# Kernel tuning notes

Measured on AMD Instinct MI355X. Metric: run time of the kernel, lower is better.

The kernel has to match this reference:

```python
import jax, jax.numpy as jnp
import numpy as np

DIM = 128
B, N = 2, 72


def setup_inputs() -> dict:
    key = jax.random.key(0)
    ks = jax.random.split(key, 6)
    s = 1.0 / np.sqrt(DIM)
    s3 = 1.0 / np.sqrt(3 * DIM)
    return {
        "node_emb": jax.random.normal(ks[0], (B * N, DIM), dtype=jnp.float32),
        "path_emb": jax.random.normal(ks[1], (B, N, N, DIM), dtype=jnp.float32),
        "W_hz": jax.random.uniform(ks[2], (DIM, DIM), minval=-s, maxval=s, dtype=jnp.float32),
        "b_hz": jax.random.uniform(ks[3], (DIM,), minval=-s, maxval=s, dtype=jnp.float32),
        "W_zz": jax.random.uniform(ks[4], (3 * DIM, DIM), minval=-s3, maxval=s3, dtype=jnp.float32),
        "b_zz": jax.random.uniform(ks[5], (DIM,), minval=-s3, maxval=s3, dtype=jnp.float32),
    }


def reference(node_emb, path_emb, W_hz, b_hz, W_zz, b_zz):
    b, n, _, d = path_emb.shape
    # z = W_hz(path_emb)
    z = jnp.einsum('bijd,de->bije', path_emb, W_hz) + b_hz
    # tropical (max-plus) triangle aggregation: out[b,i,j,d] = max_k z[b,i,k,d] + z[b,k,j,d]
    z_conv = jnp.max(z[:, :, :, None, :] + z[:, None, :, :, :], axis=2)  # (b,n,n,d)
    # path_aggr with mode 'max' -> elementwise max of z_conv and z
    z = jnp.maximum(z_conv, z)
    ne = node_emb.reshape(b, n, d)
    n_i = jnp.broadcast_to(ne[:, :, None, :], (b, n, n, d))
    n_j = jnp.broadcast_to(ne[:, None, :, :], (b, n, n, d))
    zc = jnp.concatenate([n_i, z, n_j], axis=-1)  # (b,n,n,3d)
    out = jax.nn.relu(jnp.einsum('bijc,ce->bije', zc, W_zz) + b_zz)
    return out
```

## Files before the change

kernel.cpp:

```cpp
#include <hip/hip_runtime.h>

#define DIM 128
#define NN 72
#define BB 2
#define NROWS (BB*NN*NN)
#define BN (BB*NN)
#define ZBLOCKS (NROWS/16)

__global__ __launch_bounds__(256) void k_phase1(const float* __restrict__ path,
                                                const float* __restrict__ Whz,
                                                const float* __restrict__ bhz,
                                                float* __restrict__ z,
                                                const float* __restrict__ node,
                                                const float* __restrict__ Wzz,
                                                float* __restrict__ P1,
                                                float* __restrict__ P3) {
    __shared__ float rows[16 * DIM];
    const int t = threadIdx.x;

    if (blockIdx.x < ZBLOCKS) {
        const int r0 = blockIdx.x * 16;
        {
            float4* rs = (float4*)rows;
            const float4* pg = (const float4*)(path + r0 * DIM);
            rs[t]       = pg[t];
            rs[t + 256] = pg[t + 256];
        }
        __syncthreads();

        const int e2 = t & 63;
        const int rg = t >> 6;
        float2 bz = *(const float2*)&bhz[2 * e2];
        float2 acc[4];
#pragma unroll
        for (int r = 0; r < 4; r++) acc[r] = bz;

        const float* Wp = Whz + 2 * e2;
        float2 w[4], wn[4];
#pragma unroll
        for (int dd = 0; dd < 4; dd++) w[dd] = *(const float2*)&Wp[dd * DIM];

        for (int d4 = 0; d4 < DIM / 4; d4++) {
            if (d4 < DIM / 4 - 1) {
#pragma unroll
                for (int dd = 0; dd < 4; dd++)
                    wn[dd] = *(const float2*)&Wp[(4 * d4 + 4 + dd) * DIM];
            }
            float4 pr[4];
#pragma unroll
            for (int r = 0; r < 4; r++)
                pr[r] = *(const float4*)&rows[(rg + 4 * r) * DIM + 4 * d4];
#pragma unroll
            for (int dd = 0; dd < 4; dd++)
#pragma unroll
                for (int r = 0; r < 4; r++) {
                    float pv = ((const float*)&pr[r])[dd];
                    acc[r].x = fmaf(pv, w[dd].x, acc[r].x);
                    acc[r].y = fmaf(pv, w[dd].y, acc[r].y);
                }
#pragma unroll
            for (int dd = 0; dd < 4; dd++) w[dd] = wn[dd];
        }
#pragma unroll
        for (int r = 0; r < 4; r++)
            *(float2*)&z[(r0 + rg + 4 * r) * DIM + 2 * e2] = acc[r];
    } else {
        const int r0 = (blockIdx.x - ZBLOCKS) * 8;
        {
            float4* rs = (float4*)rows;
            const float4* ng = (const float4*)(node + r0 * DIM);
            rs[t] = ng[t];
        }
        __syncthreads();
        const int e  = t & 127;
        const int rr = t >> 7;
        float a1[4] = {0.f, 0.f, 0.f, 0.f};
        float a3[4] = {0.f, 0.f, 0.f, 0.f};
        const float* W1 = Wzz + e;
        const float* W3 = Wzz + 2 * DIM * DIM + e;
        for (int d = 0; d < DIM; d++) {
            float w1 = W1[d * DIM];
            float w3 = W3[d * DIM];
#pragma unroll
            for (int s = 0; s < 4; s++) {
                float pv = rows[(rr + 2 * s) * DIM + d];
                a1[s] = fmaf(pv, w1, a1[s]);
                a3[s] = fmaf(pv, w3, a3[s]);
            }
        }
#pragma unroll
        for (int s = 0; s < 4; s++) {
            int m = r0 + rr + 2 * s;
            P1[m * DIM + e] = a1[s];
            P3[m * DIM + e] = a3[s];
        }
    }
}

__global__ __launch_bounds__(256) void k_trop(const float* __restrict__ z,
                                              float* __restrict__ zmax) {
    __shared__ float comb[16 * DIM];
    const int blk = blockIdx.x;
    const int b   = blk / 324;
    const int rem = blk - b * 324;
    const int it  = rem / 18;
    const int jt  = rem - it * 18;
    const int i0 = it * 4, j0 = jt * 4;
    const int t  = threadIdx.x;
    const int d  = t & 127;
    const int ty = t >> 7;
    const float* zb = z + b * NN * NN * DIM;

    float acc[16];
#pragma unroll
    for (int q = 0; q < 16; q++) acc[q] = -3.402823466e38f;

    float zi[4], zj[4], zin[4], zjn[4];
    int k = ty;
#pragma unroll
    for (int a = 0; a < 4; a++) zi[a] = zb[((i0 + a) * NN + k) * DIM + d];
#pragma unroll
    for (int c = 0; c < 4; c++) zj[c] = zb[(k * NN + (j0 + c)) * DIM + d];

    for (int it2 = 0; it2 < NN / 2; it2++) {
        int kn = k + 2;
        if (it2 < NN / 2 - 1) {
#pragma unroll
            for (int a = 0; a < 4; a++) zin[a] = zb[((i0 + a) * NN + kn) * DIM + d];
#pragma unroll
            for (int c = 0; c < 4; c++) zjn[c] = zb[(kn * NN + (j0 + c)) * DIM + d];
        }
#pragma unroll
        for (int a = 0; a < 4; a++)
#pragma unroll
            for (int c = 0; c < 4; c++)
                acc[a * 4 + c] = fmaxf(acc[a * 4 + c], zi[a] + zj[c]);
#pragma unroll
        for (int a = 0; a < 4; a++) { zi[a] = zin[a]; zj[a] = zjn[a]; }
        k = kn;
    }

    if (ty == 1) {
#pragma unroll
        for (int q = 0; q < 16; q++) comb[q * DIM + d] = acc[q];
    }
    __syncthreads();
    if (ty == 0) {
        float* zmb = zmax + b * NN * NN * DIM;
#pragma unroll
        for (int a = 0; a < 4; a++)
#pragma unroll
            for (int c = 0; c < 4; c++) {
                int q = a * 4 + c;
                float m = fmaxf(acc[q], comb[q * DIM + d]);
                int idx = ((i0 + a) * NN + (j0 + c)) * DIM + d;
                zmb[idx] = fmaxf(m, zb[idx]);
            }
    }
}

__global__ __launch_bounds__(256) void k_out(const float* zin,
                                             const float* __restrict__ Wzz,
                                             const float* __restrict__ bzz,
                                             const float* __restrict__ P1,
                                             const float* __restrict__ P3,
                                             float* out) {
    __shared__ float rows[16 * DIM];
    const int t  = threadIdx.x;
    const int r0 = blockIdx.x * 16;
    {
        float4* rs = (float4*)rows;
        const float4* zg = (const float4*)(zin + r0 * DIM);
        rs[t]       = zg[t];
        rs[t + 256] = zg[t + 256];
    }
    __syncthreads();

    const int e2 = t & 63;
    const int rg = t >> 6;
    float2 acc[4];
#pragma unroll
    for (int r = 0; r < 4; r++) acc[r] = make_float2(0.f, 0.f);

    const float* Wp = Wzz + DIM * DIM + 2 * e2;
    float2 w[4], wn[4];
#pragma unroll
    for (int dd = 0; dd < 4; dd++) w[dd] = *(const float2*)&Wp[dd * DIM];

    for (int d4 = 0; d4 < DIM / 4; d4++) {
        if (d4 < DIM / 4 - 1) {
#pragma unroll
            for (int dd = 0; dd < 4; dd++)
                wn[dd] = *(const float2*)&Wp[(4 * d4 + 4 + dd) * DIM];
        }
        float4 pr[4];
#pragma unroll
        for (int r = 0; r < 4; r++)
            pr[r] = *(const float4*)&rows[(rg + 4 * r) * DIM + 4 * d4];
#pragma unroll
        for (int dd = 0; dd < 4; dd++)
#pragma unroll
            for (int r = 0; r < 4; r++) {
                float pv = ((const float*)&pr[r])[dd];
                acc[r].x = fmaf(pv, w[dd].x, acc[r].x);
                acc[r].y = fmaf(pv, w[dd].y, acc[r].y);
            }
#pragma unroll
        for (int dd = 0; dd < 4; dd++) w[dd] = wn[dd];
    }

    float2 bz = *(const float2*)&bzz[2 * e2];
#pragma unroll
    for (int r = 0; r < 4; r++) {
        int row = r0 + rg + 4 * r;
        int bi  = row / NN;
        int b   = row / (NN * NN);
        int j   = row - bi * NN;
        float2 v1 = *(const float2*)&P1[bi * DIM + 2 * e2];
        float2 v3 = *(const float2*)&P3[(b * NN + j) * DIM + 2 * e2];
        float ox = fmaxf(acc[r].x + v1.x + v3.x + bz.x, 0.f);
        float oy = fmaxf(acc[r].y + v1.y + v3.y + bz.y, 0.f);
        *(float2*)&out[row * DIM + 2 * e2] = make_float2(ox, oy);
    }
}

extern "C" void kernel_launch(void* const* d_in, const int* in_sizes, int n_in,
                              void* d_out, int out_size, void* d_ws, size_t ws_size,
                              hipStream_t stream) {
    const float* node = (const float*)d_in[0];
    const float* path = (const float*)d_in[1];
    const float* Whz  = (const float*)d_in[2];
    const float* bhz  = (const float*)d_in[3];
    const float* Wzz  = (const float*)d_in[4];
    const float* bzz  = (const float*)d_in[5];
    float* out = (float*)d_out;

    float* z  = (float*)d_ws;
    float* P1 = z + NROWS * DIM;
    float* P3 = P1 + BN * DIM;
    float* zmax = out;

    hipLaunchKernelGGL(k_phase1, dim3(ZBLOCKS + 18), dim3(256), 0, stream,
                       path, Whz, bhz, z, node, Wzz, P1, P3);
    hipLaunchKernelGGL(k_trop,   dim3(BB * 18 * 18), dim3(256), 0, stream, z, zmax);
    hipLaunchKernelGGL(k_out,    dim3(ZBLOCKS),      dim3(256), 0, stream,
                       zmax, Wzz, bzz, P1, P3, out);
}
```

Before: 114.3 us.

## Fuse three kernels into one persistent kernel with a grid-wide barrier

Merges the projection, tropical max-plus aggregation and output GEMM into one kernel of 648 blocks, separated by a software grid barrier built on an atomic counter. The tropical result tile is kept in shared memory and fed straight into the output projection, so the intermediate zmax no longer goes through global memory. This also removes two kernel launch gaps. In exchange it adds a memset launch, a spin-wait barrier that needs all 648 blocks to be resident at once (launch bounds 256,3), and a deadlock risk if they are not.

```diff
diff --git a/kernel.cpp b/kernel.cpp
--- a/kernel.cpp
+++ b/kernel.cpp
@@ -5,21 +5,33 @@
 #define BB 2
 #define NROWS (BB*NN*NN)
 #define BN (BB*NN)
-#define ZBLOCKS (NROWS/16)
-
-__global__ __launch_bounds__(256) void k_phase1(const float* __restrict__ path,
-                                                const float* __restrict__ Whz,
-                                                const float* __restrict__ bhz,
-                                                float* __restrict__ z,
-                                                const float* __restrict__ node,
-                                                const float* __restrict__ Wzz,
-                                                float* __restrict__ P1,
-                                                float* __restrict__ P3) {
+#define GRID 648
+
+__device__ __forceinline__ void grid_barrier(unsigned* cnt) {
+    __syncthreads();
+    if (threadIdx.x == 0) {
+        __threadfence();
+        atomicAdd(cnt, 1u);
+        while (__hip_atomic_load(cnt, __ATOMIC_ACQUIRE,
+                                 __HIP_MEMORY_SCOPE_AGENT) < (unsigned)GRID) {}
+    }
+    __syncthreads();
+    __threadfence();
+}
+
+__global__ __launch_bounds__(256, 3) void k_fused(
+        const float* __restrict__ path, const float* __restrict__ Whz,
+        const float* __restrict__ bhz,  const float* __restrict__ node,
+        const float* __restrict__ Wzz,  const float* __restrict__ bzz,
+        float* __restrict__ z, float* __restrict__ P1, float* __restrict__ P3,
+        unsigned* cnt, float* __restrict__ out) {
     __shared__ float rows[16 * DIM];
-    const int t = threadIdx.x;
-
-    if (blockIdx.x < ZBLOCKS) {
-        const int r0 = blockIdx.x * 16;
+    __shared__ float comb[16 * DIM];
+    const int t   = threadIdx.x;
+    const int blk = blockIdx.x;
+
+    {
+        const int r0 = blk * 16;
         {
             float4* rs = (float4*)rows;
             const float4* pg = (const float4*)(path + r0 * DIM);
@@ -27,19 +39,16 @@
             rs[t + 256] = pg[t + 256];
         }
         __syncthreads();
-
         const int e2 = t & 63;
         const int rg = t >> 6;
         float2 bz = *(const float2*)&bhz[2 * e2];
         float2 acc[4];
 #pragma unroll
         for (int r = 0; r < 4; r++) acc[r] = bz;
-
         const float* Wp = Whz + 2 * e2;
         float2 w[4], wn[4];
 #pragma unroll
         for (int dd = 0; dd < 4; dd++) w[dd] = *(const float2*)&Wp[dd * DIM];
-
         for (int d4 = 0; d4 < DIM / 4; d4++) {
             if (d4 < DIM / 4 - 1) {
 #pragma unroll
@@ -64,12 +73,14 @@
 #pragma unroll
         for (int r = 0; r < 4; r++)
             *(float2*)&z[(r0 + rg + 4 * r) * DIM + 2 * e2] = acc[r];
-    } else {
-        const int r0 = (blockIdx.x - ZBLOCKS) * 8;
+    }
+
+    if (blk < 18) {
+        const int r0 = blk * 8;
         {
-            float4* rs = (float4*)rows;
+            float4* cs = (float4*)comb;
             const float4* ng = (const float4*)(node + r0 * DIM);
-            rs[t] = ng[t];
+            cs[t] = ng[t];
         }
         __syncthreads();
         const int e  = t & 127;
@@ -83,7 +94,7 @@
             float w3 = W3[d * DIM];
 #pragma unroll
             for (int s = 0; s < 4; s++) {
-                float pv = rows[(rr + 2 * s) * DIM + d];
+                float pv = comb[(rr + 2 * s) * DIM + d];
                 a1[s] = fmaf(pv, w1, a1[s]);
                 a3[s] = fmaf(pv, w3, a3[s]);
             }
@@ -95,132 +106,111 @@
             P3[m * DIM + e] = a3[s];
         }
     }
-}
-
-__global__ __launch_bounds__(256) void k_trop(const float* __restrict__ z,
-                                              float* __restrict__ zmax) {
-    __shared__ float comb[16 * DIM];
-    const int blk = blockIdx.x;
+
+    grid_barrier(cnt);
+
     const int b   = blk / 324;
     const int rem = blk - b * 324;
     const int it  = rem / 18;
     const int jt  = rem - it * 18;
     const int i0 = it * 4, j0 = jt * 4;
-    const int t  = threadIdx.x;
     const int d  = t & 127;
     const int ty = t >> 7;
     const float* zb = z + b * NN * NN * DIM;
-
-    float acc[16];
-#pragma unroll
-    for (int q = 0; q < 16; q++) acc[q] = -3.402823466e38f;
-
-    float zi[4], zj[4], zin[4], zjn[4];
-    int k = ty;
-#pragma unroll
-    for (int a = 0; a < 4; a++) zi[a] = zb[((i0 + a) * NN + k) * DIM + d];
-#pragma unroll
-    for (int c = 0; c < 4; c++) zj[c] = zb[(k * NN + (j0 + c)) * DIM + d];
-
-    for (int it2 = 0; it2 < NN / 2; it2++) {
-        int kn = k + 2;
-        if (it2 < NN / 2 - 1) {
-#pragma unroll
-            for (int a = 0; a < 4; a++) zin[a] = zb[((i0 + a) * NN + kn) * DIM + d];
-#pragma unroll
-            for (int c = 0; c < 4; c++) zjn[c] = zb[(kn * NN + (j0 + c)) * DIM + d];
-        }
-#pragma unroll
-        for (int a = 0; a < 4; a++)
-#pragma unroll
-            for (int c = 0; c < 4; c++)
-                acc[a * 4 + c] = fmaxf(acc[a * 4 + c], zi[a] + zj[c]);
-#pragma unroll
-        for (int a = 0; a < 4; a++) { zi[a] = zin[a]; zj[a] = zjn[a]; }
-        k = kn;
-    }
-
-    if (ty == 1) {
-#pragma unroll
-        for (int q = 0; q < 16; q++) comb[q * DIM + d] = acc[q];
+    {
+        float acc[16];
+#pragma unroll
+        for (int q = 0; q < 16; q++) acc[q] = -3.402823466e38f;
+
+        float zi[4], zj[4], zin[4], zjn[4];
+        int k = ty;
+#pragma unroll
+        for (int a = 0; a < 4; a++) zi[a] = zb[((i0 + a) * NN + k) * DIM + d];
+#pragma unroll
+        for (int c = 0; c < 4; c++) zj[c] = zb[(k * NN + (j0 + c)) * DIM + d];
+
+        for (int it2 = 0; it2 < NN / 2; it2++) {
+            int kn = k + 2;
+            if (it2 < NN / 2 - 1) {
+#pragma unroll
+                for (int a = 0; a < 4; a++) zin[a] = zb[((i0 + a) * NN + kn) * DIM + d];
+#pragma unroll
+                for (int c = 0; c < 4; c++) zjn[c] = zb[(kn * NN + (j0 + c)) * DIM + d];
+            }
+#pragma unroll
+            for (int a = 0; a < 4; a++)
+#pragma unroll
+                for (int c = 0; c < 4; c++)
+                    acc[a * 4 + c] = fmaxf(acc[a * 4 + c], zi[a] + zj[c]);
+#pragma unroll
+            for (int a = 0; a < 4; a++) { zi[a] = zin[a]; zj[a] = zjn[a]; }
+            k = kn;
+        }
+
+        if (ty == 1) {
+#pragma unroll
+            for (int q = 0; q < 16; q++) comb[q * DIM + d] = acc[q];
+        }
+        __syncthreads();
+        if (ty == 0) {
+#pragma unroll
+            for (int a = 0; a < 4; a++)
+#pragma unroll
+                for (int c = 0; c < 4; c++) {
+                    int q = a * 4 + c;
+                    float m = fmaxf(acc[q], comb[q * DIM + d]);
+                    int idx = ((i0 + a) * NN + (j0 + c)) * DIM + d;
+                    rows[q * DIM + d] = fmaxf(m, zb[idx]);
+                }
+        }
     }
     __syncthreads();
-    if (ty == 0) {
-        float* zmb = zmax + b * NN * NN * DIM;
-#pragma unroll
-        for (int a = 0; a < 4; a++)
-#pragma unroll
-            for (int c = 0; c < 4; c++) {
-                int q = a * 4 + c;
-                float m = fmaxf(acc[q], comb[q * DIM + d]);
-                int idx = ((i0 + a) * NN + (j0 + c)) * DIM + d;
-                zmb[idx] = fmaxf(m, zb[idx]);
-            }
-    }
-}
-
-__global__ __launch_bounds__(256) void k_out(const float* zin,
-                                             const float* __restrict__ Wzz,
-                                             const float* __restrict__ bzz,
-                                             const float* __restrict__ P1,
-                                             const float* __restrict__ P3,
-                                             float* out) {
-    __shared__ float rows[16 * DIM];
-    const int t  = threadIdx.x;
-    const int r0 = blockIdx.x * 16;
+
     {
-        float4* rs = (float4*)rows;
-        const float4* zg = (const float4*)(zin + r0 * DIM);
-        rs[t]       = zg[t];
-        rs[t + 256] = zg[t + 256];
-    }
-    __syncthreads();
-
-    const int e2 = t & 63;
-    const int rg = t >> 6;
-    float2 acc[4];
-#pragma unroll
-    for (int r = 0; r < 4; r++) acc[r] = make_float2(0.f, 0.f);
-
-    const float* Wp = Wzz + DIM * DIM + 2 * e2;
-    float2 w[4], wn[4];
-#pragma unroll
-    for (int dd = 0; dd < 4; dd++) w[dd] = *(const float2*)&Wp[dd * DIM];
-
-    for (int d4 = 0; d4 < DIM / 4; d4++) {
-        if (d4 < DIM / 4 - 1) {
+        const int e2 = t & 63;
+        const int rg = t >> 6;
+        float2 acc[4];
+#pragma unroll
+        for (int r = 0; r < 4; r++) acc[r] = make_float2(0.f, 0.f);
+
+        const float* Wp = Wzz + DIM * DIM + 2 * e2;
+        float2 w[4], wn[4];
+#pragma unroll
+        for (int dd = 0; dd < 4; dd++) w[dd] = *(const float2*)&Wp[dd * DIM];
+        for (int d4 = 0; d4 < DIM / 4; d4++) {
+            if (d4 < DIM / 4 - 1) {
+#pragma unroll
+                for (int dd = 0; dd < 4; dd++)
+                    wn[dd] = *(const float2*)&Wp[(4 * d4 + 4 + dd) * DIM];
+            }
+            float4 pr[4];
+#pragma unroll
+            for (int r = 0; r < 4; r++)
+                pr[r] = *(const float4*)&rows[(rg + 4 * r) * DIM + 4 * d4];
 #pragma unroll
             for (int dd = 0; dd < 4; dd++)
-                wn[dd] = *(const float2*)&Wp[(4 * d4 + 4 + dd) * DIM];
-        }
-        float4 pr[4];
-#pragma unroll
-        for (int r = 0; r < 4; r++)
-            pr[r] = *(const float4*)&rows[(rg + 4 * r) * DIM + 4 * d4];
-#pragma unroll
-        for (int dd = 0; dd < 4; dd++)
-#pragma unroll
-            for (int r = 0; r < 4; r++) {
-                float pv = ((const float*)&pr[r])[dd];
-                acc[r].x = fmaf(pv, w[dd].x, acc[r].x);
-                acc[r].y = fmaf(pv, w[dd].y, acc[r].y);
-            }
-#pragma unroll
-        for (int dd = 0; dd < 4; dd++) w[dd] = wn[dd];
-    }
-
-    float2 bz = *(const float2*)&bzz[2 * e2];
-#pragma unroll
-    for (int r = 0; r < 4; r++) {
-        int row = r0 + rg + 4 * r;
-        int bi  = row / NN;
-        int b   = row / (NN * NN);
-        int j   = row - bi * NN;
-        float2 v1 = *(const float2*)&P1[bi * DIM + 2 * e2];
-        float2 v3 = *(const float2*)&P3[(b * NN + j) * DIM + 2 * e2];
-        float ox = fmaxf(acc[r].x + v1.x + v3.x + bz.x, 0.f);
-        float oy = fmaxf(acc[r].y + v1.y + v3.y + bz.y, 0.f);
-        *(float2*)&out[row * DIM + 2 * e2] = make_float2(ox, oy);
+#pragma unroll
+                for (int r = 0; r < 4; r++) {
+                    float pv = ((const float*)&pr[r])[dd];
+                    acc[r].x = fmaf(pv, w[dd].x, acc[r].x);
+                    acc[r].y = fmaf(pv, w[dd].y, acc[r].y);
+                }
+#pragma unroll
+            for (int dd = 0; dd < 4; dd++) w[dd] = wn[dd];
+        }
+
+        float2 bz = *(const float2*)&bzz[2 * e2];
+#pragma unroll
+        for (int r = 0; r < 4; r++) {
+            int q = rg + 4 * r;
+            int a = q >> 2, c = q & 3;
+            int orow = b * NN * NN + (i0 + a) * NN + (j0 + c);
+            float2 v1 = *(const float2*)&P1[(b * NN + i0 + a) * DIM + 2 * e2];
+            float2 v3 = *(const float2*)&P3[(b * NN + j0 + c) * DIM + 2 * e2];
+            float ox = fmaxf(acc[r].x + v1.x + v3.x + bz.x, 0.f);
+            float oy = fmaxf(acc[r].y + v1.y + v3.y + bz.y, 0.f);
+            *(float2*)&out[orow * DIM + 2 * e2] = make_float2(ox, oy);
+        }
     }
 }
 
@@ -235,14 +225,13 @@
     const float* bzz  = (const float*)d_in[5];
     float* out = (float*)d_out;
 
-    float* z  = (float*)d_ws;
+    unsigned* cnt = (unsigned*)d_ws;
+    float* base = (float*)d_ws;
+    float* z  = base + 256;
     float* P1 = z + NROWS * DIM;
     float* P3 = P1 + BN * DIM;
-    float* zmax = out;
-
-    hipLaunchKernelGGL(k_phase1, dim3(ZBLOCKS + 18), dim3(256), 0, stream,
-                       path, Whz, bhz, z, node, Wzz, P1, P3);
-    hipLaunchKernelGGL(k_trop,   dim3(BB * 18 * 18), dim3(256), 0, stream, z, zmax);
-    hipLaunchKernelGGL(k_out,    dim3(ZBLOCKS),      dim3(256), 0, stream,
-                       zmax, Wzz, bzz, P1, P3, out);
+
+    hipMemsetAsync(d_ws, 0, 64, stream);
+    hipLaunchKernelGGL(k_fused, dim3(GRID), dim3(256), 0, stream,
+                       path, Whz, bhz, node, Wzz, bzz, z, P1, P3, cnt, out);
 }
```

Measured after the change: 325.8 us. 2.85x slower.
